# Kernel optimization log

Hardware: AMD Instinct MI355X
Metric: run time of the kernel (lower is better)

Reference implementation:

```python
import jax, jax.numpy as jnp
import numpy as np

BS, NQ, NV, E = 8, 1000, 20000, 256
HH, DH, L, P, FFN = 8, 32, 1, 4, 512
SPATIAL = ((100, 200),)  # (H, W) per level; sum(H*W) == NV


def layer_norm(x, w, b):
    mu = jnp.mean(x, -1, keepdims=True)
    var = jnp.mean((x - mu) ** 2, -1, keepdims=True)
    return (x - mu) / jnp.sqrt(var + 1e-5) * w + b


def mha(q_in, k_in, v_in, in_w, in_b, out_w, out_b):
    # q_in/k_in/v_in: (len, BS, E), batch_first=False semantics of nn.MultiheadAttention
    Wq, Wk, Wv = jnp.split(in_w, 3, axis=0)
    bq, bk, bv = jnp.split(in_b, 3, axis=0)
    def heads(x, W, b):  # (len,B,E) -> (B,HH,len,DH)
        y = x @ W.T + b
        return y.reshape(y.shape[0], BS, HH, DH).transpose(1, 2, 0, 3)
    q = heads(q_in, Wq, bq) / jnp.sqrt(jnp.asarray(DH, q_in.dtype))
    k = heads(k_in, Wk, bk)
    v = heads(v_in, Wv, bv)
    attn = jax.nn.softmax(jnp.einsum('bhqd,bhkd->bhqk', q, k), axis=-1)
    o = jnp.einsum('bhqk,bhkd->bhqd', attn, v)  # (B,HH,Lq,DH)
    o = o.transpose(2, 0, 1, 3).reshape(-1, BS, E)
    return o @ out_w.T + out_b


def bilinear_sample(img, grid):
    # img: (B,H,W,C); grid: (B,NQ,P,2) in [-1,1]; align_corners=False, zero padding
    B, H, W, C = img.shape
    x = (grid[..., 0] + 1.0) * 0.5 * W - 0.5
    y = (grid[..., 1] + 1.0) * 0.5 * H - 0.5
    x0 = jnp.floor(x); y0 = jnp.floor(y)
    wx = x - x0; wy = y - y0
    flat = img.reshape(B, H * W, C)
    def gather(xi, yi):
        valid = (xi >= 0) & (xi < W) & (yi >= 0) & (yi < H)
        xc = jnp.clip(xi, 0, W - 1).astype(jnp.int32)
        yc = jnp.clip(yi, 0, H - 1).astype(jnp.int32)
        idx = (yc * W + xc).reshape(B, -1, 1)
        v = jnp.take_along_axis(flat, idx, axis=1).reshape(*xi.shape, C)
        return v * valid[..., None].astype(img.dtype)
    v00 = gather(x0, y0); v01 = gather(x0 + 1, y0)
    v10 = gather(x0, y0 + 1); v11 = gather(x0 + 1, y0 + 1)
    wx = wx[..., None]; wy = wy[..., None]
    return (v00 * (1 - wx) * (1 - wy) + v01 * wx * (1 - wy)
            + v10 * (1 - wx) * wy + v11 * wx * wy)


def msda(value, sampling_locations, attention_weights):
    # value: (BS,NV,HH,DH); locations: (BS,NQ,HH,L,P,2); weights: (BS,NQ,HH,L,P)
    grids = 2.0 * sampling_locations - 1.0
    start = 0
    outs = []
    for lvl, (H, W) in enumerate(SPATIAL):
        v = value[:, start:start + H * W]           # (BS,HW,HH,DH)
        start += H * W
        img = v.transpose(0, 2, 1, 3).reshape(BS * HH, H, W, DH)
        g = grids[:, :, :, lvl].transpose(0, 2, 1, 3, 4).reshape(BS * HH, NQ, P, 2)
        outs.append(bilinear_sample(img, g))        # (BS*HH,NQ,P,DH)
    sampled = jnp.stack(outs, axis=2)               # (BS*HH,NQ,L,P,DH)
    aw = attention_weights.transpose(0, 2, 1, 3, 4).reshape(BS * HH, NQ, L, P)
    out = jnp.einsum('bqlpd,bqlp->bqd', sampled, aw)
    return out.reshape(BS, HH, NQ, DH).transpose(0, 2, 1, 3).reshape(BS, NQ, E)


def setup_inputs() -> dict:
    key = jax.random.key(0)
    ks = jax.random.split(key, 24)
    s = 1.0 / np.sqrt(E)
    # sampling_offsets bias: torch init grid (circular directions scaled by point idx)
    th = np.arange(HH, dtype=np.float32) * (2.0 * np.pi / HH)
    grid = np.stack([np.cos(th), np.sin(th)], -1)
    grid = grid / np.abs(grid).max(-1, keepdims=True)
    grid = np.tile(grid[:, None, None, :], (1, L, P, 1)) * np.arange(1, P + 1, dtype=np.float32)[None, None, :, None]
    return {
        'query': jax.random.normal(ks[0], (NQ, BS, E), jnp.float32),
        'query_pos': jax.random.normal(ks[1], (NQ, BS, E), jnp.float32),
        'value': jax.random.normal(ks[2], (NV, BS, E), jnp.float32),
        'reference_points': jax.random.uniform(ks[3], (BS, NQ, L, 2), jnp.float32),
        'in_proj_w': jax.random.normal(ks[4], (3 * E, E), jnp.float32) * s,
        'in_proj_b': jnp.zeros((3 * E,), jnp.float32),
        'out_proj_w': jax.random.normal(ks[5], (E, E), jnp.float32) * s,
        'out_proj_b': jnp.zeros((E,), jnp.float32),
        'ln1_w': jnp.ones((E,), jnp.float32), 'ln1_b': jnp.zeros((E,), jnp.float32),
        'ln2_w': jnp.ones((E,), jnp.float32), 'ln2_b': jnp.zeros((E,), jnp.float32),
        'ln3_w': jnp.ones((E,), jnp.float32), 'ln3_b': jnp.zeros((E,), jnp.float32),
        'off_w': jax.random.normal(ks[6], (HH * L * P * 2, E), jnp.float32) * 0.01,
        'off_b': jnp.asarray(grid.reshape(-1)),
        'aw_w': jax.random.normal(ks[7], (HH * L * P, E), jnp.float32) * 0.01,
        'aw_b': jnp.zeros((HH * L * P,), jnp.float32),
        'vproj_w': jax.random.normal(ks[8], (E, E), jnp.float32) * s,
        'vproj_b': jnp.zeros((E,), jnp.float32),
        'oproj_w': jax.random.normal(ks[9], (E, E), jnp.float32) * s,
        'oproj_b': jnp.zeros((E,), jnp.float32),
        'ffn_w1': jax.random.normal(ks[10], (FFN, E), jnp.float32) * s,
        'ffn_b1': jnp.zeros((FFN,), jnp.float32),
        'ffn_w2': jax.random.normal(ks[11], (E, FFN), jnp.float32) / np.sqrt(FFN),
        'ffn_b2': jnp.zeros((E,), jnp.float32),
    }


def reference(query, query_pos, value, reference_points,
              in_proj_w, in_proj_b, out_proj_w, out_proj_b,
              ln1_w, ln1_b, ln2_w, ln2_b, ln3_w, ln3_b,
              off_w, off_b, aw_w, aw_b, vproj_w, vproj_b, oproj_w, oproj_b,
              ffn_w1, ffn_b1, ffn_w2, ffn_b2):
    # --- self-attn: q=k=query+pos, v=query; residual inside; dropout=eval (identity)
    qp = query + query_pos
    x = layer_norm(query + mha(qp, qp, query, in_proj_w, in_proj_b, out_proj_w, out_proj_b), ln1_w, ln1_b)
    # --- deformable cross-attn ---
    xq_b = (x + query_pos).transpose(1, 0, 2)         # (BS,NQ,E)
    v = (value.transpose(1, 0, 2) @ vproj_w.T + vproj_b).reshape(BS, NV, HH, DH)
    off = (xq_b @ off_w.T + off_b).reshape(BS, NQ, HH, L, P, 2)
    aw = jax.nn.softmax((xq_b @ aw_w.T + aw_b).reshape(BS, NQ, HH, L * P), -1).reshape(BS, NQ, HH, L, P)
    norm = jnp.asarray([[w, h] for (h, w) in SPATIAL], jnp.float32)  # (L,2) = (W,H)
    loc = reference_points[:, :, None, :, None, :] + off / norm[None, None, None, :, None, :]
    ms = msda(v, loc, aw) @ oproj_w.T + oproj_b       # (BS,NQ,E)
    x = layer_norm(x + ms.transpose(1, 0, 2), ln2_w, ln2_b)
    # --- FFN ---
    h = jnp.maximum(x @ ffn_w1.T + ffn_b1, 0.0)
    return layer_norm(x + h @ ffn_w2.T + ffn_b2, ln3_w, ln3_b)
```

## Files before the change

### kernel.cpp

```cpp
#include <hip/hip_runtime.h>
#include <hip/hip_bf16.h>
#include <cmath>

constexpr int cBS = 8;
constexpr int cNQ = 1000;
constexpr int cNV = 20000;
constexpr int cE  = 256;
constexpr int cHH = 8;
constexpr int cDH = 32;
constexpr int cP  = 4;
constexpr int cFFN = 512;
constexpr int cH = 100;
constexpr int cW = 200;
constexpr int NTOK = cNQ * cBS;
constexpr size_t QKSZ2 = (size_t)64 * 1024 * cDH;

typedef float f32x4 __attribute__((ext_vector_type(4)));
typedef short bf16x8 __attribute__((ext_vector_type(8)));
union U8 { uint u[4]; bf16x8 v; };

__device__ __forceinline__ void split_bf(float x, ushort& h, ushort& l) {
    __hip_bfloat16 hb = __float2bfloat16(x);
    float hf = __bfloat162float(hb);
    __hip_bfloat16 lb = __float2bfloat16(x - hf);
    h = *reinterpret_cast<ushort*>(&hb);
    l = *reinterpret_cast<ushort*>(&lb);
}
__device__ __forceinline__ void pk_split2(float a, float b, uint& h, uint& l) {
    __hip_bfloat16 ah = __float2bfloat16(a), bh = __float2bfloat16(b);
    float arf = a - __bfloat162float(ah), brf = b - __bfloat162float(bh);
    __hip_bfloat16 al = __float2bfloat16(arf), bl = __float2bfloat16(brf);
    h = ((uint)*reinterpret_cast<ushort*>(&bh) << 16) | *reinterpret_cast<ushort*>(&ah);
    l = ((uint)*reinterpret_cast<ushort*>(&bl) << 16) | *reinterpret_cast<ushort*>(&al);
}

__device__ __forceinline__ void gl_lds16(const float* g, float* l) {
    __builtin_amdgcn_global_load_lds(
        (const __attribute__((address_space(1))) unsigned int*)g,
        (__attribute__((address_space(3))) unsigned int*)l,
        16, 0, 0);
}

__global__ __launch_bounds__(256) void k_zerou4(uint4* __restrict__ p, int n)
{
    int i = blockIdx.x * 256 + threadIdx.x;
    if (i < n) p[i] = uint4{0u, 0u, 0u, 0u};
}

__global__ __launch_bounds__(256) void k_prepw(
    const float* __restrict__ Wsrc, ushort* __restrict__ wpk,
    int nkk , int total , int losz )
{
    int gid = blockIdx.x * 256 + threadIdx.x;
    if (gid >= total) return;
    int g  = gid & 3;
    int kk = (gid >> 2) % nkk;
    int n  = gid / (4 * nkk);
    const float* src = Wsrc + (size_t)n * (nkk * 32) + kk * 32 + 4 * g;
    float4 x0 = *reinterpret_cast<const float4*>(src);
    float4 x1 = *reinterpret_cast<const float4*>(src + 16);
    float xs[8] = {x0.x, x0.y, x0.z, x0.w, x1.x, x1.y, x1.z, x1.w};
    union { ushort s[8]; uint4 q; } hi_, lo_;
#pragma unroll
    for (int j = 0; j < 8; j++) split_bf(xs[j], hi_.s[j], lo_.s[j]);
    *reinterpret_cast<uint4*>(wpk + (size_t)gid * 8)        = hi_.q;
    *reinterpret_cast<uint4*>(wpk + losz + (size_t)gid * 8) = lo_.q;
}

__global__ __launch_bounds__(256) void k_prepw2(
    const float* __restrict__ Wsrc, ushort* __restrict__ wpk)
{
    int gid = blockIdx.x * 256 + threadIdx.x;
    if (gid >= 8192) return;
    int lane = gid & 63;
    int kk   = (gid >> 6) & 7;
    int nblk = gid >> 9;
    int ln = lane & 15, g = lane >> 4;
    int n = ((nblk >> 2) << 6) + (ln << 2) + (nblk & 3);
    const float* src = Wsrc + (size_t)n * cE + kk * 32 + 4 * g;
    float4 x0 = *reinterpret_cast<const float4*>(src);
    float4 x1 = *reinterpret_cast<const float4*>(src + 16);
    float xs[8] = {x0.x, x0.y, x0.z, x0.w, x1.x, x1.y, x1.z, x1.w};
    union { ushort s[8]; uint4 q; } hi_, lo_;
#pragma unroll
    for (int j = 0; j < 8; j++) split_bf(xs[j], hi_.s[j], lo_.s[j]);
    *reinterpret_cast<uint4*>(wpk + (size_t)gid * 8)         = hi_.q;
    *reinterpret_cast<uint4*>(wpk + 65536 + (size_t)gid * 8) = lo_.q;
}

__global__ __launch_bounds__(256) void k_bgemm2(
    const float* __restrict__ A, const ushort* __restrict__ wpk2,
    const float* __restrict__ bias, float* __restrict__ vimg)
{
    __shared__ float lds[2][2048];
    const int t    = threadIdx.x;
    const int w    = t >> 6;
    const int lane = t & 63;
    const int g    = lane >> 4;
    const int ln   = lane & 15;
    const int bm   = blockIdx.x * 64;
    const ushort* wlo = wpk2 + 65536;

    f32x4 acc[4][4];
#pragma unroll
    for (int mt = 0; mt < 4; mt++)
#pragma unroll
        for (int nt = 0; nt < 4; nt++) acc[mt][nt] = {0.f, 0.f, 0.f, 0.f};

#define VSTAGE(buf, kkv) {                                                          \
    int row0_ = (w << 4) + (lane >> 3);                                             \
    int c0_ = ((lane & 7) << 4) ^ ((row0_ & 7) << 4);                               \
    gl_lds16(A + (size_t)(bm + row0_) * cE + (kkv) * 32 + (c0_ >> 2),               \
             &lds[buf][(w << 9)]);                                                  \
    int row1_ = row0_ + 8;                                                          \
    int c1_ = ((lane & 7) << 4) ^ ((row1_ & 7) << 4);                               \
    gl_lds16(A + (size_t)(bm + row1_) * cE + (kkv) * 32 + (c1_ >> 2),               \
             &lds[buf][(w << 9) + 256]);                                            \
}

    VSTAGE(0, 0)
    __syncthreads();

#pragma unroll
    for (int kk = 0; kk < 8; kk++) {
        const int cur = kk & 1;
        if (kk < 7) VSTAGE(cur ^ 1, kk + 1)

        U8 wh[4], wl[4];
#pragma unroll
        for (int nt = 0; nt < 4; nt++) {
            size_t off = (((size_t)(w * 4 + nt) * 8 + kk) * 64 + lane) * 8;
            *reinterpret_cast<uint4*>(&wh[nt].u[0]) = *reinterpret_cast<const uint4*>(wpk2 + off);
            *reinterpret_cast<uint4*>(&wl[nt].u[0]) = *reinterpret_cast<const uint4*>(wlo + off);
        }

        const char* lb = (const char*)(&lds[cur][0]);
#pragma unroll
        for (int mt = 0; mt < 4; mt++) {
            int row = mt * 16 + ln;
            int mk = (row & 7) << 4;
            float4 x0 = *reinterpret_cast<const float4*>(lb + row * 128 + ((g * 16) ^ mk));
            float4 x1 = *reinterpret_cast<const float4*>(lb + row * 128 + ((64 + g * 16) ^ mk));
            float xs[8] = {x0.x, x0.y, x0.z, x0.w, x1.x, x1.y, x1.z, x1.w};
            U8 aH, aL;
            union { ushort s[8]; uint u[4]; } hs, ls;
#pragma unroll
            for (int j = 0; j < 8; j++) split_bf(xs[j], hs.s[j], ls.s[j]);
#pragma unroll
            for (int i = 0; i < 4; i++) { aH.u[i] = hs.u[i]; aL.u[i] = ls.u[i]; }
#pragma unroll
            for (int nt = 0; nt < 4; nt++) {
                acc[mt][nt] = __builtin_amdgcn_mfma_f32_16x16x32_bf16(aL.v, wh[nt].v, acc[mt][nt], 0, 0, 0);
                acc[mt][nt] = __builtin_amdgcn_mfma_f32_16x16x32_bf16(aH.v, wl[nt].v, acc[mt][nt], 0, 0, 0);
                acc[mt][nt] = __builtin_amdgcn_mfma_f32_16x16x32_bf16(aH.v, wh[nt].v, acc[mt][nt], 0, 0, 0);
            }
        }
        __syncthreads();
    }
#undef VSTAGE

    const int cb = w * 64 + ln * 4;
    float4 bv4 = *reinterpret_cast<const float4*>(&bias[cb]);
#pragma unroll
    for (int mt = 0; mt < 4; mt++) {
#pragma unroll
        for (int r = 0; r < 4; r++) {
            int gr = bm + mt * 16 + 4 * g + r;
            float4 o;
            o.x = acc[mt][0][r] + bv4.x;
            o.y = acc[mt][1][r] + bv4.y;
            o.z = acc[mt][2][r] + bv4.z;
            o.w = acc[mt][3][r] + bv4.w;
            *reinterpret_cast<float4*>(&vimg[(size_t)gr * cE + cb]) = o;
        }
    }
}

__global__ __launch_bounds__(256) void k_oagemm(
    const float* __restrict__ xq, const ushort* __restrict__ wpk,
    float* __restrict__ raw)
{
    const int w    = threadIdx.x >> 6;
    const int lane = threadIdx.x & 63;
    const int g    = lane >> 4;
    const int ln   = lane & 15;
    const int row0 = blockIdx.x * 64 + w * 16;
    const ushort* wlo = wpk + 24576;

    f32x4 acc[6];
#pragma unroll
    for (int nt = 0; nt < 6; nt++) acc[nt] = {0.f, 0.f, 0.f, 0.f};

    for (int kk = 0; kk < 8; kk++) {
        const float* ap = xq + (size_t)(row0 + ln) * cE + kk * 32 + 4 * g;
        float4 u0 = *reinterpret_cast<const float4*>(ap);
        float4 u1 = *reinterpret_cast<const float4*>(ap + 16);
        float xs[8] = {u0.x, u0.y, u0.z, u0.w, u1.x, u1.y, u1.z, u1.w};
        U8 aH, aL;
        union { ushort s[8]; uint u[4]; } hs, ls;
#pragma unroll
        for (int j = 0; j < 8; j++) split_bf(xs[j], hs.s[j], ls.s[j]);
#pragma unroll
        for (int i = 0; i < 4; i++) { aH.u[i] = hs.u[i]; aL.u[i] = ls.u[i]; }
#pragma unroll
        for (int nt = 0; nt < 6; nt++) {
            int n = nt * 16 + ln;
            size_t off = ((size_t)(n * 8 + kk) * 4 + g) * 8;
            U8 wh, wl;
            *reinterpret_cast<uint4*>(&wh.u[0]) = *reinterpret_cast<const uint4*>(wpk + off);
            *reinterpret_cast<uint4*>(&wl.u[0]) = *reinterpret_cast<const uint4*>(wlo + off);
            acc[nt] = __builtin_amdgcn_mfma_f32_16x16x32_bf16(aL.v, wh.v, acc[nt], 0, 0, 0);
            acc[nt] = __builtin_amdgcn_mfma_f32_16x16x32_bf16(aH.v, wl.v, acc[nt], 0, 0, 0);
            acc[nt] = __builtin_amdgcn_mfma_f32_16x16x32_bf16(aH.v, wh.v, acc[nt], 0, 0, 0);
        }
    }

#pragma unroll
    for (int nt = 0; nt < 6; nt++) {
        int n = nt * 16 + ln;
#pragma unroll
        for (int r = 0; r < 4; r++) {
            int row = row0 + 4 * g + r;
            raw[(size_t)row * 96 + n] = acc[nt][r];
        }
    }
}

__global__ __launch_bounds__(256) void k_locaw(
    const float* __restrict__ raw, const float* __restrict__ offb,
    const float* __restrict__ awbias, const float* __restrict__ refp,
    float* __restrict__ locO, float* __restrict__ awO)
{
    int gid = blockIdx.x * 256 + threadIdx.x;
    if (gid >= NTOK * 96) return;
    int i = gid % 96;
    int tok = gid / 96;
    int q = tok >> 3, b = tok & 7;
    int bq = b * cNQ + q;
    const float* rr = raw + (size_t)tok * 96;
    if (i < 64) {
        int c = i & 1;
        float offv = rr[i] + offb[i];
        float refv = refp[((size_t)b * cNQ + q) * 2 + c];
        float nrm = (c == 0) ? 200.f : 100.f;
        locO[(size_t)bq * 64 + i] = refv + offv / nrm;
    } else {
        int j = i - 64;
        int gbase = j & ~3;
        float x0 = rr[64 + gbase + 0] + awbias[gbase + 0];
        float x1 = rr[64 + gbase + 1] + awbias[gbase + 1];
        float x2 = rr[64 + gbase + 2] + awbias[gbase + 2];
        float x3 = rr[64 + gbase + 3] + awbias[gbase + 3];
        float xm = rr[64 + j] + awbias[j];
        float mx = fmaxf(fmaxf(x0, x1), fmaxf(x2, x3));
        float e = __expf(xm - mx);
        float ssum = __expf(x0 - mx) + __expf(x1 - mx) + __expf(x2 - mx) + __expf(x3 - mx);
        awO[(size_t)bq * 32 + j] = e / ssum;
    }
}

constexpr int MM_QKV   = 1;
constexpr int MM_PLAIN = 2;
constexpr int MM_RELU  = 3;
constexpr int MM_OPROJ = 4;

template <int MODE, int TKK, int NFULL>
__global__ __launch_bounds__(256) void k_mgemm(
    const float* __restrict__ A, const float* __restrict__ A2,
    const ushort* __restrict__ wpk, int losz,
    const float* __restrict__ bias,
    void* __restrict__ C0, void* __restrict__ C1, void* __restrict__ C2)
{
    const int w    = threadIdx.x >> 6;
    const int lane = threadIdx.x & 63;
    const int g    = lane >> 4;
    const int ln   = lane & 15;
    const int bm   = blockIdx.x * 32;
    const int slab = blockIdx.y;
    const int nb   = slab * 256 + w * 64;
    const ushort* wlo = wpk + losz;
    const int K = TKK * 32;

    f32x4 acc[2][4];
#pragma unroll
    for (int mt = 0; mt < 2; mt++)
#pragma unroll
        for (int nt = 0; nt < 4; nt++) acc[mt][nt] = {0.f, 0.f, 0.f, 0.f};

    U8 wh[2][4], wl[2][4];
    float ax[2][2][8];

#define MG_LOADW(kk, buf) {                                                        \
    _Pragma("unroll")                                                              \
    for (int nt = 0; nt < 4; nt++) {                                               \
        int n = nb + nt * 16 + ln;                                                 \
        size_t off = ((size_t)(n * TKK + (kk)) * 4 + g) * 8;                       \
        *reinterpret_cast<uint4*>(&wh[buf][nt].u[0]) = *reinterpret_cast<const uint4*>(wpk + off); \
        *reinterpret_cast<uint4*>(&wl[buf][nt].u[0]) = *reinterpret_cast<const uint4*>(wlo + off); \
    } }

#define MG_LOADA(kk, buf) {                                                        \
    _Pragma("unroll")                                                              \
    for (int mt = 0; mt < 2; mt++) {                                               \
        const float* ap = A + (size_t)(bm + mt * 16 + ln) * K + (kk) * 32 + 4 * g; \
        float4 u0 = *reinterpret_cast<const float4*>(ap);                          \
        float4 u1 = *reinterpret_cast<const float4*>(ap + 16);                     \
        if (MODE == MM_QKV && slab < 2) {                                          \
            const float* bp = A2 + (size_t)(bm + mt * 16 + ln) * K + (kk) * 32 + 4 * g; \
            float4 v0 = *reinterpret_cast<const float4*>(bp);                      \
            float4 v1 = *reinterpret_cast<const float4*>(bp + 16);                 \
            u0.x += v0.x; u0.y += v0.y; u0.z += v0.z; u0.w += v0.w;                \
            u1.x += v1.x; u1.y += v1.y; u1.z += v1.z; u1.w += v1.w;                \
        }                                                                          \
        ax[buf][mt][0] = u0.x; ax[buf][mt][1] = u0.y;                              \
        ax[buf][mt][2] = u0.z; ax[buf][mt][3] = u0.w;                              \
        ax[buf][mt][4] = u1.x; ax[buf][mt][5] = u1.y;                              \
        ax[buf][mt][6] = u1.z; ax[buf][mt][7] = u1.w;                              \
    } }

#define MG_STEP(buf) {                                                             \
    _Pragma("unroll")                                                              \
    for (int mt = 0; mt < 2; mt++) {                                               \
        U8 aH, aL;                                                                 \
        union { ushort s[8]; uint u[4]; } hs, ls;                                  \
        _Pragma("unroll")                                                          \
        for (int j = 0; j < 8; j++) split_bf(ax[buf][mt][j], hs.s[j], ls.s[j]);    \
        _Pragma("unroll")                                                          \
        for (int i = 0; i < 4; i++) { aH.u[i] = hs.u[i]; aL.u[i] = ls.u[i]; }      \
        _Pragma("unroll")                                                          \
        for (int nt = 0; nt < 4; nt++) {                                           \
            acc[mt][nt] = __builtin_amdgcn_mfma_f32_16x16x32_bf16(aL.v, wh[buf][nt].v, acc[mt][nt], 0, 0, 0); \
            acc[mt][nt] = __builtin_amdgcn_mfma_f32_16x16x32_bf16(aH.v, wl[buf][nt].v, acc[mt][nt], 0, 0, 0); \
            acc[mt][nt] = __builtin_amdgcn_mfma_f32_16x16x32_bf16(aH.v, wh[buf][nt].v, acc[mt][nt], 0, 0, 0); \
        }                                                                          \
    } }

    MG_LOADW(0, 0)
    MG_LOADA(0, 0)
#pragma unroll
    for (int kk = 0; kk < TKK; kk++) {
        if (kk + 1 < TKK) {
            MG_LOADW(kk + 1, (kk + 1) & 1)
            MG_LOADA(kk + 1, (kk + 1) & 1)
        }
        MG_STEP(kk & 1)
    }
#undef MG_LOADW
#undef MG_LOADA
#undef MG_STEP

#pragma unroll
    for (int nt = 0; nt < 4; nt++) {
        int n = nb + nt * 16 + ln;
        float bv = bias[n];
#pragma unroll
        for (int mt = 0; mt < 2; mt++) {
#pragma unroll
            for (int r = 0; r < 4; r++) {
                int gr = bm + mt * 16 + 4 * g + r;
                float val = acc[mt][nt][r] + bv;
                if (MODE == MM_QKV) {
                    int tok = gr >> 3, b = gr & 7;
                    int nloc = n & 255, h = nloc >> 5, d = nloc & 31;
                    if (slab == 0) val *= 0.17677669529663687f;
                    ushort hs, ls;
                    split_bf(val, hs, ls);
                    if (slab < 2) {
                        int slot = ((d >> 2) & 3) * 8 + (d & 3) + 4 * (d >> 4);
                        ushort* base = (slab == 0) ? (ushort*)C0 : (ushort*)C1;
                        size_t off = ((size_t)(b * cHH + h) * 1024 + tok) * 32 + slot;
                        base[off]         = hs;
                        base[QKSZ2 + off] = ls;
                    } else {
                        int o = tok & 31, kbi = tok >> 5;
                        int slot = ((o >> 2) & 3) * 8 + (o & 3) + 4 * (o >> 4);
                        ushort* vb = (ushort*)C2;
                        size_t off = ((size_t)(b * cHH + h) * 32 + d) * 1024 + kbi * 32 + slot;
                        vb[off]         = hs;
                        vb[QKSZ2 + off] = ls;
                    }
                } else if (MODE == MM_OPROJ) {
                    int b = gr / cNQ, q = gr - b * cNQ;
                    ((float*)C0)[((size_t)q * cBS + b) * cE + n] = val;
                } else {
                    if (MODE == MM_RELU) val = fmaxf(val, 0.f);
                    ((float*)C0)[(size_t)gr * NFULL + n] = val;
                }
            }
        }
    }
}

__global__ __launch_bounds__(256) void k_attn3(
    const ushort* __restrict__ qhi, const ushort* __restrict__ qlo,
    const ushort* __restrict__ khi, const ushort* __restrict__ klo,
    const ushort* __restrict__ vhi, const ushort* __restrict__ vlo,
    float* __restrict__ po, float* __restrict__ plsum)
{
    const int bid   = blockIdx.x;
    const int xcd   = bid & 7;
    const int inner = bid >> 3;
    const int bh    = ((inner & 7) << 3) + xcd;
    const int rest  = inner >> 3;
    const int qbix  = rest & 7;
    const int z     = rest >> 3;

    const int w    = threadIdx.x >> 6;
    const int lane = threadIdx.x & 63;
    const int g    = lane >> 4;
    const int ql   = lane & 15;
    const int qA   = qbix * 128 + w * 32;

    const size_t qoffA = ((size_t)bh * 1024 + qA + ql) * 32 + g * 8;
    U8 bQAh, bQAl, bQBh, bQBl;
    *reinterpret_cast<uint4*>(&bQAh.u[0]) = *reinterpret_cast<const uint4*>(qhi + qoffA);
    *reinterpret_cast<uint4*>(&bQAl.u[0]) = *reinterpret_cast<const uint4*>(qlo + qoffA);
    *reinterpret_cast<uint4*>(&bQBh.u[0]) = *reinterpret_cast<const uint4*>(qhi + qoffA + 16 * 32);
    *reinterpret_cast<uint4*>(&bQBl.u[0]) = *reinterpret_cast<const uint4*>(qlo + qoffA + 16 * 32);
    const size_t koff = ((size_t)bh * 1024 + ql) * 32 + g * 8;
    const size_t voff = ((size_t)bh * 32 + ql) * 1024 + g * 8;

    f32x4 oA0 = {0.f,0.f,0.f,0.f}, oA1 = {0.f,0.f,0.f,0.f};
    f32x4 oB0 = {0.f,0.f,0.f,0.f}, oB1 = {0.f,0.f,0.f,0.f};
    float lpartA = 0.f, lpartB = 0.f;
    const f32x4 zz = {0.f, 0.f, 0.f, 0.f};

    const int kt0 = z * 16;
#pragma unroll
    for (int kti = 0; kti < 16; kti++) {
        const int kt = kt0 + kti;
        U8 k0h, k1h, k0l, k1l, v0h, v1h, v0l, v1l;
        {
            size_t kb32 = (size_t)kt * 32 * 32;
            *reinterpret_cast<uint4*>(&k0h.u[0]) = *reinterpret_cast<const uint4*>(khi + koff + kb32);
            *reinterpret_cast<uint4*>(&k1h.u[0]) = *reinterpret_cast<const uint4*>(khi + koff + kb32 + 512);
            *reinterpret_cast<uint4*>(&k0l.u[0]) = *reinterpret_cast<const uint4*>(klo + koff + kb32);
            *reinterpret_cast<uint4*>(&k1l.u[0]) = *reinterpret_cast<const uint4*>(klo + koff + kb32 + 512);
            size_t vb32 = voff + (size_t)kt * 32;
            *reinterpret_cast<uint4*>(&v0h.u[0]) = *reinterpret_cast<const uint4*>(vhi + vb32);
            *reinterpret_cast<uint4*>(&v1h.u[0]) = *reinterpret_cast<const uint4*>(vhi + vb32 + 16 * 1024);
            *reinterpret_cast<uint4*>(&v0l.u[0]) = *reinterpret_cast<const uint4*>(vlo + vb32);
            *reinterpret_cast<uint4*>(&v1l.u[0]) = *reinterpret_cast<const uint4*>(vlo + vb32 + 16 * 1024);
        }

        const bool tail = (kti == 15) && (z == 1);

        f32x4 sA0 = __builtin_amdgcn_mfma_f32_16x16x32_bf16(k0l.v, bQAh.v, zz, 0, 0, 0);
        sA0 = __builtin_amdgcn_mfma_f32_16x16x32_bf16(k0h.v, bQAl.v, sA0, 0, 0, 0);
        sA0 = __builtin_amdgcn_mfma_f32_16x16x32_bf16(k0h.v, bQAh.v, sA0, 0, 0, 0);
        f32x4 sB0 = __builtin_amdgcn_mfma_f32_16x16x32_bf16(k0l.v, bQBh.v, zz, 0, 0, 0);
        sB0 = __builtin_amdgcn_mfma_f32_16x16x32_bf16(k0h.v, bQBl.v, sB0, 0, 0, 0);
        sB0 = __builtin_amdgcn_mfma_f32_16x16x32_bf16(k0h.v, bQBh.v, sB0, 0, 0, 0);
        f32x4 sA1, sB1;
        if (tail) {
            int tb = 31 * 32 + 4 * g;
#pragma unroll
            for (int r = 0; r < 4; r++) {
                if (tb + r >= cNQ) { sA0[r] = -INFINITY; sB0[r] = -INFINITY; }
            }
            sA1[0] = sA1[1] = sA1[2] = sA1[3] = -INFINITY;
            sB1[0] = sB1[1] = sB1[2] = sB1[3] = -INFINITY;
        } else {
            sA1 = __builtin_amdgcn_mfma_f32_16x16x32_bf16(k1l.v, bQAh.v, zz, 0, 0, 0);
            sA1 = __builtin_amdgcn_mfma_f32_16x16x32_bf16(k1h.v, bQAl.v, sA1, 0, 0, 0);
            sA1 = __builtin_amdgcn_mfma_f32_16x16x32_bf16(k1h.v, bQAh.v, sA1, 0, 0, 0);
            sB1 = __builtin_amdgcn_mfma_f32_16x16x32_bf16(k1l.v, bQBh.v, zz, 0, 0, 0);
            sB1 = __builtin_amdgcn_mfma_f32_16x16x32_bf16(k1h.v, bQBl.v, sB1, 0, 0, 0);
            sB1 = __builtin_amdgcn_mfma_f32_16x16x32_bf16(k1h.v, bQBh.v, sB1, 0, 0, 0);
        }

        float pA00 = __expf(sA0[0]), pA01 = __expf(sA0[1]);
        float pA02 = __expf(sA0[2]), pA03 = __expf(sA0[3]);
        float pA10 = __expf(sA1[0]), pA11 = __expf(sA1[1]);
        float pA12 = __expf(sA1[2]), pA13 = __expf(sA1[3]);
        lpartA += ((pA00 + pA01) + (pA02 + pA03)) + ((pA10 + pA11) + (pA12 + pA13));
        float pB00 = __expf(sB0[0]), pB01 = __expf(sB0[1]);
        float pB02 = __expf(sB0[2]), pB03 = __expf(sB0[3]);
        float pB10 = __expf(sB1[0]), pB11 = __expf(sB1[1]);
        float pB12 = __expf(sB1[2]), pB13 = __expf(sB1[3]);
        lpartB += ((pB00 + pB01) + (pB02 + pB03)) + ((pB10 + pB11) + (pB12 + pB13));

        U8 fpAh, fpAl, fpBh, fpBl;
        pk_split2(pA00, pA01, fpAh.u[0], fpAl.u[0]);
        pk_split2(pA02, pA03, fpAh.u[1], fpAl.u[1]);
        pk_split2(pA10, pA11, fpAh.u[2], fpAl.u[2]);
        pk_split2(pA12, pA13, fpAh.u[3], fpAl.u[3]);
        pk_split2(pB00, pB01, fpBh.u[0], fpBl.u[0]);
        pk_split2(pB02, pB03, fpBh.u[1], fpBl.u[1]);
        pk_split2(pB10, pB11, fpBh.u[2], fpBl.u[2]);
        pk_split2(pB12, pB13, fpBh.u[3], fpBl.u[3]);

        oA0 = __builtin_amdgcn_mfma_f32_16x16x32_bf16(v0l.v, fpAh.v, oA0, 0, 0, 0);
        oA0 = __builtin_amdgcn_mfma_f32_16x16x32_bf16(v0h.v, fpAl.v, oA0, 0, 0, 0);
        oA0 = __builtin_amdgcn_mfma_f32_16x16x32_bf16(v0h.v, fpAh.v, oA0, 0, 0, 0);
        oA1 = __builtin_amdgcn_mfma_f32_16x16x32_bf16(v1l.v, fpAh.v, oA1, 0, 0, 0);
        oA1 = __builtin_amdgcn_mfma_f32_16x16x32_bf16(v1h.v, fpAl.v, oA1, 0, 0, 0);
        oA1 = __builtin_amdgcn_mfma_f32_16x16x32_bf16(v1h.v, fpAh.v, oA1, 0, 0, 0);
        oB0 = __builtin_amdgcn_mfma_f32_16x16x32_bf16(v0l.v, fpBh.v, oB0, 0, 0, 0);
        oB0 = __builtin_amdgcn_mfma_f32_16x16x32_bf16(v0h.v, fpBl.v, oB0, 0, 0, 0);
        oB0 = __builtin_amdgcn_mfma_f32_16x16x32_bf16(v0h.v, fpBh.v, oB0, 0, 0, 0);
        oB1 = __builtin_amdgcn_mfma_f32_16x16x32_bf16(v1l.v, fpBh.v, oB1, 0, 0, 0);
        oB1 = __builtin_amdgcn_mfma_f32_16x16x32_bf16(v1h.v, fpBl.v, oB1, 0, 0, 0);
        oB1 = __builtin_amdgcn_mfma_f32_16x16x32_bf16(v1h.v, fpBh.v, oB1, 0, 0, 0);
    }

    float lsumA = lpartA;
    lsumA += __shfl_xor(lsumA, 16, 64);
    lsumA += __shfl_xor(lsumA, 32, 64);
    float lsumB = lpartB;
    lsumB += __shfl_xor(lsumB, 16, 64);
    lsumB += __shfl_xor(lsumB, 32, 64);

    {
        const int q = qA + ql;
        if (q < cNQ) {
            size_t base = ((size_t)(z * 64 + bh) * 1000 + q) * 32;
            float4 v0, v1;
            v0.x = oA0[0]; v0.y = oA0[1]; v0.z = oA0[2]; v0.w = oA0[3];
            v1.x = oA1[0]; v1.y = oA1[1]; v1.z = oA1[2]; v1.w = oA1[3];
            *reinterpret_cast<float4*>(po + base + 4 * g)      = v0;
            *reinterpret_cast<float4*>(po + base + 16 + 4 * g) = v1;
            if (g == 0) plsum[(size_t)(z * 64 + bh) * 1000 + q] = lsumA;
        }
    }
    {
        const int q = qA + 16 + ql;
        if (q < cNQ) {
            size_t base = ((size_t)(z * 64 + bh) * 1000 + q) * 32;
            float4 v0, v1;
            v0.x = oB0[0]; v0.y = oB0[1]; v0.z = oB0[2]; v0.w = oB0[3];
            v1.x = oB1[0]; v1.y = oB1[1]; v1.z = oB1[2]; v1.w = oB1[3];
            *reinterpret_cast<float4*>(po + base + 4 * g)      = v0;
            *reinterpret_cast<float4*>(po + base + 16 + 4 * g) = v1;
            if (g == 0) plsum[(size_t)(z * 64 + bh) * 1000 + q] = lsumB;
        }
    }
}

__global__ __launch_bounds__(256) void k_ared(
    const float* __restrict__ po, const float* __restrict__ plsum,
    float* __restrict__ outp)
{
    int gid = blockIdx.x * 256 + threadIdx.x;
    if (gid >= 64 * 1000 * 32) return;
    int d   = gid & 31;
    int rem = gid >> 5;
    int q   = rem % 1000;
    int bh  = rem / 1000;
    float o = po[gid] + po[(size_t)64 * 1000 * 32 + gid];
    float l = plsum[rem] + plsum[64000 + rem];
    int b = bh >> 3, h = bh & 7;
    outp[((size_t)q * cBS + b) * cE + h * 32 + d] = o / l;
}

__global__ __launch_bounds__(256) void k_ln(
    const float* __restrict__ a, const float* __restrict__ b,
    const float* __restrict__ w, const float* __restrict__ bias,
    const float* __restrict__ addc,
    float* __restrict__ outp, float* __restrict__ out2)
{
    int rrow = blockIdx.x, t = threadIdx.x;
    size_t base = (size_t)rrow * cE;
    float v = a[base + t] + b[base + t];
    float s = v;
#pragma unroll
    for (int off = 32; off > 0; off >>= 1) s += __shfl_down(s, off, 64);
    __shared__ float red1[4], red2[4];
    int wid = t >> 6, lane = t & 63;
    if (lane == 0) red1[wid] = s;
    __syncthreads();
    float mu = (red1[0] + red1[1] + red1[2] + red1[3]) * (1.f / cE);
    float e = v - mu;
    float s2 = e * e;
#pragma unroll
    for (int off = 32; off > 0; off >>= 1) s2 += __shfl_down(s2, off, 64);
    if (lane == 0) red2[wid] = s2;
    __syncthreads();
    float var = (red2[0] + red2[1] + red2[2] + red2[3]) * (1.f / cE);
    float y = e * (1.f / sqrtf(var + 1e-5f)) * w[t] + bias[t];
    outp[base + t] = y;
    if (out2 != nullptr) out2[base + t] = y + addc[base + t];
}

__device__ __forceinline__ float samp_one(const float* __restrict__ img, int x, int y)
{
    bool ok = (x >= 0) & (x < cW) & (y >= 0) & (y < cH);
    int xc = min(max(x, 0), cW - 1);
    int yc = min(max(y, 0), cH - 1);
    float v = img[(size_t)(yc * cW + xc) * (cBS * cE)];
    return ok ? v : 0.f;
}

__global__ __launch_bounds__(256) void k_msda(
    const float* __restrict__ vimg, const float* __restrict__ loc,
    const float* __restrict__ aw, float* __restrict__ msp)
{
    int gid = blockIdx.x * 256 + threadIdx.x;
    int d  = gid & 31;
    int h  = (gid >> 5) & 7;
    int bq = gid >> 8;
    int b  = bq / cNQ;
    const float* lp = loc + ((size_t)bq * cHH + h) * (cP * 2);
    const float* ap = aw + ((size_t)bq * cHH + h) * cP;
    const float* img = vimg + (size_t)b * cE + h * cDH + d;
    float acc = 0.f;
#pragma unroll
    for (int p = 0; p < cP; p++) {
        float g0 = 2.f * lp[p * 2 + 0] - 1.f;
        float g1 = 2.f * lp[p * 2 + 1] - 1.f;
        float xf = (g0 + 1.f) * 0.5f * (float)cW - 0.5f;
        float yf = (g1 + 1.f) * 0.5f * (float)cH - 0.5f;
        float x0f = floorf(xf), y0f = floorf(yf);
        float wx = xf - x0f, wy = yf - y0f;
        int x0 = (int)x0f, y0 = (int)y0f;
        float v00 = samp_one(img, x0,     y0);
        float v01 = samp_one(img, x0 + 1, y0);
        float v10 = samp_one(img, x0,     y0 + 1);
        float v11 = samp_one(img, x0 + 1, y0 + 1);
        float bil = v00 * (1.f - wx) * (1.f - wy) + v01 * wx * (1.f - wy)
                  + v10 * (1.f - wx) * wy        + v11 * wx * wy;
        acc = fmaf(bil, ap[p], acc);
    }
    msp[gid] = acc;
}

extern "C" void kernel_launch(void* const* d_in, const int* in_sizes, int n_in,
                              void* d_out, int out_size, void* d_ws, size_t ws_size,
                              hipStream_t stream)
{
    const float* query = (const float*)d_in[0];
    const float* qpos  = (const float*)d_in[1];
    const float* value = (const float*)d_in[2];
    const float* refp  = (const float*)d_in[3];
    const float* inw   = (const float*)d_in[4];
    const float* inb   = (const float*)d_in[5];
    const float* outw  = (const float*)d_in[6];
    const float* outb  = (const float*)d_in[7];
    const float* ln1w  = (const float*)d_in[8];
    const float* ln1b  = (const float*)d_in[9];
    const float* ln2w  = (const float*)d_in[10];
    const float* ln2b  = (const float*)d_in[11];
    const float* ln3w  = (const float*)d_in[12];
    const float* ln3b  = (const float*)d_in[13];
    const float* offw  = (const float*)d_in[14];
    const float* offb  = (const float*)d_in[15];
    const float* aww   = (const float*)d_in[16];
    const float* awbias= (const float*)d_in[17];
    const float* vpw   = (const float*)d_in[18];
    const float* vpb   = (const float*)d_in[19];
    const float* opw   = (const float*)d_in[20];
    const float* opb   = (const float*)d_in[21];
    const float* f1w   = (const float*)d_in[22];
    const float* f1b   = (const float*)d_in[23];
    const float* f2w   = (const float*)d_in[24];
    const float* f2b   = (const float*)d_in[25];
    float* out = (float*)d_out;

    float* ws = (float*)d_ws;
    const size_t S = (size_t)NTOK * cE;
    const size_t BPADF = 6 * QKSZ2 / 2;
    const size_t WPKF = 655360 + 24576;
    const size_t PLS  = 128000;
    const size_t need = 2 * S + BPADF + 512000 + 256000 + WPKF + PLS + (size_t)cBS * cHH * cNV * cDH;
    if (ws_size < need * sizeof(float)) return;

    float* P0   = ws;
    float* P1   = ws + S;
    float* Bpad = ws + 2 * S;
    float* locb = Bpad + BPADF;
    float* awb2 = locb + 512000;
    float* wpkf = awb2 + 256000;
    float* plsb = wpkf + WPKF;
    float* vimg = plsb + PLS;

    ushort* qhi = (ushort*)Bpad;
    ushort* qlo = qhi + QKSZ2;
    ushort* khi = qhi + 2 * QKSZ2;
    ushort* klo = qhi + 3 * QKSZ2;
    ushort* vhi = qhi + 4 * QKSZ2;
    ushort* vlo = qhi + 5 * QKSZ2;

    ushort* wpk_vp = (ushort*)wpkf;
    ushort* wpk_in = wpk_vp + 131072;
    ushort* wpk_ou = wpk_in + 393216;
    ushort* wpk_op = wpk_ou + 131072;
    ushort* wpk_f1 = wpk_op + 131072;
    ushort* wpk_f2 = wpk_f1 + 262144;
    ushort* wpk_oa = wpk_f2 + 262144;

    k_prepw2<<<dim3(32), dim3(256), 0, stream>>>(vpw, wpk_vp);
    k_prepw<<<dim3(96), dim3(256), 0, stream>>>(inw,  wpk_in, 8,  24576, 196608);
    k_prepw<<<dim3(32), dim3(256), 0, stream>>>(outw, wpk_ou, 8,  8192,  65536);
    k_prepw<<<dim3(32), dim3(256), 0, stream>>>(opw,  wpk_op, 8,  8192,  65536);
    k_prepw<<<dim3(64), dim3(256), 0, stream>>>(f1w,  wpk_f1, 8,  16384, 131072);
    k_prepw<<<dim3(64), dim3(256), 0, stream>>>(f2w,  wpk_f2, 16, 16384, 131072);
    k_prepw<<<dim3(8),  dim3(256), 0, stream>>>(offw, wpk_oa, 8,  2048,  24576);
    k_prepw<<<dim3(4),  dim3(256), 0, stream>>>(aww,  wpk_oa + 16384, 8, 1024, 24576);

    k_bgemm2<<<dim3(2500), dim3(256), 0, stream>>>(value, wpk_vp, vpb, vimg);

    k_zerou4<<<dim3(2048), dim3(256), 0, stream>>>(
        reinterpret_cast<uint4*>(vhi), (int)(2 * QKSZ2 * 2 / 16));

    k_mgemm<MM_QKV, 8, 768><<<dim3(250, 3), dim3(256), 0, stream>>>(
        query, qpos, wpk_in, 196608, inb, qhi, khi, vhi);

    k_attn3<<<dim3(1024), dim3(256), 0, stream>>>(
        qhi, qlo, khi, klo, vhi, vlo, P0, plsb);

    float* attn_pre = Bpad;
    k_ared<<<dim3(8000), dim3(256), 0, stream>>>(P0, plsb, attn_pre);

    float* mha_y = P1;
    k_mgemm<MM_PLAIN, 8, 256><<<dim3(250, 1), dim3(256), 0, stream>>>(
        attn_pre, nullptr, wpk_ou, 65536, outb, mha_y, nullptr, nullptr);

    float* x  = Bpad;
    float* xq = Bpad + S;
    k_ln<<<dim3(NTOK), dim3(256), 0, stream>>>(query, mha_y, ln1w, ln1b, qpos, x, xq);

    float* rawb = P0;
    k_oagemm<<<dim3(125), dim3(256), 0, stream>>>(xq, wpk_oa, rawb);
    k_locaw<<<dim3((NTOK * 96 + 255) / 256), dim3(256), 0, stream>>>(
        rawb, offb, awbias, refp, locb, awb2);

    float* ms_pre = P1;
    k_msda<<<dim3(NTOK * cE / 256), dim3(256), 0, stream>>>(vimg, locb, awb2, ms_pre);

    float* ms_y = P0;
    k_mgemm<MM_OPROJ, 8, 256><<<dim3(250, 1), dim3(256), 0, stream>>>(
        ms_pre, nullptr, wpk_op, 65536, opb, ms_y, nullptr, nullptr);

    float* x2 = Bpad + 2 * S;
    k_ln<<<dim3(NTOK), dim3(256), 0, stream>>>(x, ms_y, ln2w, ln2b, nullptr, x2, nullptr);

    float* hbuf = Bpad;
    k_mgemm<MM_RELU, 8, 512><<<dim3(250, 2), dim3(256), 0, stream>>>(
        x2, nullptr, wpk_f1, 131072, f1b, hbuf, nullptr, nullptr);
    float* y3 = P0;
    k_mgemm<MM_PLAIN, 16, 256><<<dim3(250, 1), dim3(256), 0, stream>>>(
        hbuf, nullptr, wpk_f2, 131072, f2b, y3, nullptr, nullptr);

    k_ln<<<dim3(NTOK), dim3(256), 0, stream>>>(x2, y3, ln3w, ln3b, nullptr, out, nullptr);
}
```

Before: 409.6 us.

## Fuse split-KV attention reduction into out-proj GEMM and shrink V zeroing

Removes the separate k_ared kernel by having the out-projection GEMM's A-load combine the two split-KV partial outputs and normalize by the summed lse directly, avoiding a round trip through a global intermediate. The full zeroing of the padded V buffer is replaced by a small kernel that zeros only the padding tail rows. Risks: the GEMM A-load now does strided gathers across head layouts and a division per row, and correctness relies on only the last 32-row block needing zeros.

```diff
diff --git a/kernel.cpp b/kernel.cpp
--- a/kernel.cpp
+++ b/kernel.cpp
@@ -41,10 +41,18 @@
         16, 0, 0);
 }
 
-__global__ __launch_bounds__(256) void k_zerou4(uint4* __restrict__ p, int n)
+__global__ __launch_bounds__(256) void k_zerovpad(ushort* __restrict__ vhi)
 {
     int i = blockIdx.x * 256 + threadIdx.x;
-    if (i < n) p[i] = uint4{0u, 0u, 0u, 0u};
+    if (i >= 4096) return;
+    int bhd = i & 2047;
+    int buf = i >> 11;
+    ushort* p = vhi + (size_t)buf * QKSZ2 + (size_t)bhd * 1024 + 31 * 32;
+    uint4 z = {0u, 0u, 0u, 0u};
+    *reinterpret_cast<uint4*>(p)      = z;
+    *reinterpret_cast<uint4*>(p + 8)  = z;
+    *reinterpret_cast<uint4*>(p + 16) = z;
+    *reinterpret_cast<uint4*>(p + 24) = z;
 }
 
 __global__ __launch_bounds__(256) void k_prepw(
@@ -263,6 +271,7 @@
 constexpr int MM_PLAIN = 2;
 constexpr int MM_RELU  = 3;
 constexpr int MM_OPROJ = 4;
+constexpr int MM_ARED  = 5;
 
 template <int MODE, int TKK, int NFULL>
 __global__ __launch_bounds__(256) void k_mgemm(
@@ -302,15 +311,35 @@
 #define MG_LOADA(kk, buf) {                                                        \
     _Pragma("unroll")                                                              \
     for (int mt = 0; mt < 2; mt++) {                                               \
-        const float* ap = A + (size_t)(bm + mt * 16 + ln) * K + (kk) * 32 + 4 * g; \
-        float4 u0 = *reinterpret_cast<const float4*>(ap);                          \
-        float4 u1 = *reinterpret_cast<const float4*>(ap + 16);                     \
-        if (MODE == MM_QKV && slab < 2) {                                          \
-            const float* bp = A2 + (size_t)(bm + mt * 16 + ln) * K + (kk) * 32 + 4 * g; \
-            float4 v0 = *reinterpret_cast<const float4*>(bp);                      \
-            float4 v1 = *reinterpret_cast<const float4*>(bp + 16);                 \
-            u0.x += v0.x; u0.y += v0.y; u0.z += v0.z; u0.w += v0.w;                \
-            u1.x += v1.x; u1.y += v1.y; u1.z += v1.z; u1.w += v1.w;                \
+        float4 u0, u1;                                                             \
+        if (MODE == MM_ARED) {                                                     \
+            int gr = bm + mt * 16 + ln;                                            \
+            int q = gr >> 3, b = gr & 7;                                           \
+            int bh0 = (b << 3) + (kk);       \
+            size_t r0 = ((size_t)bh0 * 1000 + q) * 32;                             \
+            const float* p0 = A + r0;                                              \
+            const float* p1 = A + 2048000 + r0;                                    \
+            float4 a0 = *reinterpret_cast<const float4*>(p0 + 4 * g);              \
+            float4 c0 = *reinterpret_cast<const float4*>(p1 + 4 * g);              \
+            float4 a1 = *reinterpret_cast<const float4*>(p0 + 16 + 4 * g);         \
+            float4 c1 = *reinterpret_cast<const float4*>(p1 + 16 + 4 * g);         \
+            float l = A2[(size_t)bh0 * 1000 + q] + A2[64000 + (size_t)bh0 * 1000 + q]; \
+            float rl = 1.f / l;                                                    \
+            u0.x = (a0.x + c0.x) * rl; u0.y = (a0.y + c0.y) * rl;                  \
+            u0.z = (a0.z + c0.z) * rl; u0.w = (a0.w + c0.w) * rl;                  \
+            u1.x = (a1.x + c1.x) * rl; u1.y = (a1.y + c1.y) * rl;                  \
+            u1.z = (a1.z + c1.z) * rl; u1.w = (a1.w + c1.w) * rl;                  \
+        } else {                                                                   \
+            const float* ap = A + (size_t)(bm + mt * 16 + ln) * K + (kk) * 32 + 4 * g; \
+            u0 = *reinterpret_cast<const float4*>(ap);                             \
+            u1 = *reinterpret_cast<const float4*>(ap + 16);                        \
+            if (MODE == MM_QKV && slab < 2) {                                      \
+                const float* bp = A2 + (size_t)(bm + mt * 16 + ln) * K + (kk) * 32 + 4 * g; \
+                float4 v0 = *reinterpret_cast<const float4*>(bp);                  \
+                float4 v1 = *reinterpret_cast<const float4*>(bp + 16);             \
+                u0.x += v0.x; u0.y += v0.y; u0.z += v0.z; u0.w += v0.w;            \
+                u1.x += v1.x; u1.y += v1.y; u1.z += v1.z; u1.w += v1.w;            \
+            }                                                                      \
         }                                                                          \
         ax[buf][mt][0] = u0.x; ax[buf][mt][1] = u0.y;                              \
         ax[buf][mt][2] = u0.z; ax[buf][mt][3] = u0.w;                              \
@@ -537,22 +566,6 @@
     }
 }
 
-__global__ __launch_bounds__(256) void k_ared(
-    const float* __restrict__ po, const float* __restrict__ plsum,
-    float* __restrict__ outp)
-{
-    int gid = blockIdx.x * 256 + threadIdx.x;
-    if (gid >= 64 * 1000 * 32) return;
-    int d   = gid & 31;
-    int rem = gid >> 5;
-    int q   = rem % 1000;
-    int bh  = rem / 1000;
-    float o = po[gid] + po[(size_t)64 * 1000 * 32 + gid];
-    float l = plsum[rem] + plsum[64000 + rem];
-    int b = bh >> 3, h = bh & 7;
-    outp[((size_t)q * cBS + b) * cE + h * 32 + d] = o / l;
-}
-
 __global__ __launch_bounds__(256) void k_ln(
     const float* __restrict__ a, const float* __restrict__ b,
     const float* __restrict__ w, const float* __restrict__ bias,
@@ -699,8 +712,7 @@
 
     k_bgemm2<<<dim3(2500), dim3(256), 0, stream>>>(value, wpk_vp, vpb, vimg);
 
-    k_zerou4<<<dim3(2048), dim3(256), 0, stream>>>(
-        reinterpret_cast<uint4*>(vhi), (int)(2 * QKSZ2 * 2 / 16));
+    k_zerovpad<<<dim3(16), dim3(256), 0, stream>>>(vhi);
 
     k_mgemm<MM_QKV, 8, 768><<<dim3(250, 3), dim3(256), 0, stream>>>(
         query, qpos, wpk_in, 196608, inb, qhi, khi, vhi);
@@ -708,12 +720,9 @@
     k_attn3<<<dim3(1024), dim3(256), 0, stream>>>(
         qhi, qlo, khi, klo, vhi, vlo, P0, plsb);
 
-    float* attn_pre = Bpad;
-    k_ared<<<dim3(8000), dim3(256), 0, stream>>>(P0, plsb, attn_pre);
-
     float* mha_y = P1;
-    k_mgemm<MM_PLAIN, 8, 256><<<dim3(250, 1), dim3(256), 0, stream>>>(
-        attn_pre, nullptr, wpk_ou, 65536, outb, mha_y, nullptr, nullptr);
+    k_mgemm<MM_ARED, 8, 256><<<dim3(250, 1), dim3(256), 0, stream>>>(
+        P0, plsb, wpk_ou, 65536, outb, mha_y, nullptr, nullptr);
 
     float* x  = Bpad;
     float* xq = Bpad + S;
```

New measurement: 408.8 us. About the same (-0.2%).
